# Optimization experiments

Measured on AMD Instinct MI355X. Metric: run time of the kernel, lower is better.

Reference implementation:

```python
import jax, jax.numpy as jnp
import numpy as np
from jax import lax

D, H, DK, L, FF, V, B, S = 384, 12, 32, 6, 1536, 30522, 16, 512

def _logit(p):
    return float(np.log(p / (1.0 - p)))

def setup_inputs():
    key = jax.random.key(0)
    ks = jax.random.split(key, 16)
    def g(i, shape, scale=0.02):
        return jax.random.normal(ks[i], shape, jnp.float32) * scale
    return {
        "input_ids": jax.random.randint(ks[0], (B, S), 0, V),
        "attention_mask": jnp.ones((B, S), jnp.int32),
        "emb_tok": g(1, (V, D)),
        "emb_pos": g(2, (S, D)),
        "emb_type": g(3, (2, D)),
        "emb_ln_g": jnp.ones((D,), jnp.float32),
        "emb_ln_b": jnp.zeros((D,), jnp.float32),
        "Wq": g(4, (L, D, D)), "bq": jnp.zeros((L, D), jnp.float32),
        "Wk": g(5, (L, D, D)), "bk": jnp.zeros((L, D), jnp.float32),
        "Wv": g(6, (L, D, D)), "bv": jnp.zeros((L, D), jnp.float32),
        "Wbeta": g(7, (L, D, H)), "bbeta": jnp.zeros((L, H), jnp.float32),
        "decay_fast": jnp.full((L, H), _logit(0.3), jnp.float32),
        "decay_slow": jnp.full((L, H), _logit(0.85), jnp.float32),
        "mix_logit": jnp.zeros((L, H), jnp.float32),
        "Wg": g(8, (L, D, D)),
        "Wo": g(9, (L, D, D)), "bo": jnp.zeros((L, D), jnp.float32),
        "attn_ln_g": jnp.ones((L, D), jnp.float32), "attn_ln_b": jnp.zeros((L, D), jnp.float32),
        "Wffn1": g(10, (L, D, FF)), "bffn1": jnp.zeros((L, FF), jnp.float32),
        "Wffn2": g(11, (L, FF, D)), "bffn2": jnp.zeros((L, D), jnp.float32),
        "ffn_ln_g": jnp.ones((L, D), jnp.float32), "ffn_ln_b": jnp.zeros((L, D), jnp.float32),
    }

def _ln(x, g, b, eps=1e-12):
    m = x.mean(-1, keepdims=True)
    v = ((x - m) ** 2).mean(-1, keepdims=True)
    return (x - m) * lax.rsqrt(v + eps) * g + b

def _delta_attn(x, mask_f, Wq, bq, Wk, bk, Wv, bv, Wbeta, bbeta, df_logit, ds_logit, mix_logit, Wg, Wo, bo):
    # Hierarchical delta-rule linear attention: O(n) recurrence, two decay timescales.
    Bz, Sq, _ = x.shape
    q = jax.nn.silu((x @ Wq + bq).reshape(Bz, Sq, H, DK))
    k = jax.nn.silu((x @ Wk + bk).reshape(Bz, Sq, H, DK))
    k = k / (jnp.linalg.norm(k, axis=-1, keepdims=True) + 1e-6)
    v = (x @ Wv + bv).reshape(Bz, Sq, H, DK)
    beta = jax.nn.sigmoid(x @ Wbeta + bbeta) * mask_f[..., None]  # [B,S,H]
    df = jax.nn.sigmoid(df_logit)[None, :, None, None]  # fast decay, per head
    ds = jax.nn.sigmoid(ds_logit)[None, :, None, None]  # slow decay, per head
    qT = q.transpose(1, 0, 2, 3)  # time-major [S,B,H,DK]
    kT = k.transpose(1, 0, 2, 3)
    vT = v.transpose(1, 0, 2, 3)
    betaT = beta.transpose(1, 0, 2)

    def step(carry, xs):
        Sf, Ss = carry  # [B,H,DK,DK] fast/slow memory states
        kt, vt, qt, bt = xs
        err_f = (vt - jnp.einsum('bhk,bhkv->bhv', kt, Sf)) * bt[..., None]
        Sf = df * Sf + jnp.einsum('bhk,bhv->bhkv', kt, err_f)
        err_s = (vt - jnp.einsum('bhk,bhkv->bhv', kt, Ss)) * bt[..., None]
        Ss = ds * Ss + jnp.einsum('bhk,bhv->bhkv', kt, err_s)
        of = jnp.einsum('bhk,bhkv->bhv', qt, Sf)
        os = jnp.einsum('bhk,bhkv->bhv', qt, Ss)
        return (Sf, Ss), (of, os)

    S0 = jnp.zeros((Bz, H, DK, DK), x.dtype)
    _, (ofT, osT) = lax.scan(step, (S0, S0), (kT, vT, qT, betaT))
    mix = jax.nn.sigmoid(mix_logit)[None, None, :, None]
    o = mix * ofT.transpose(1, 0, 2, 3) + (1.0 - mix) * osT.transpose(1, 0, 2, 3)
    o = o.reshape(Bz, Sq, D)
    o = o * jax.nn.sigmoid(x @ Wg)  # enhanced-flux output gate
    return o @ Wo + bo

def reference(input_ids, attention_mask, emb_tok, emb_pos, emb_type, emb_ln_g, emb_ln_b, Wq, bq, Wk, bk, Wv, bv, Wbeta, bbeta, decay_fast, decay_slow, mix_logit, Wg, Wo, bo, attn_ln_g, attn_ln_b, Wffn1, bffn1, Wffn2, bffn2, ffn_ln_g, ffn_ln_b):
    mask_f = attention_mask.astype(jnp.float32)
    h = emb_tok[input_ids] + emb_pos[None, :input_ids.shape[1]] + emb_type[0][None, None]
    h = _ln(h, emb_ln_g, emb_ln_b)
    for i in range(L):
        attn = _delta_attn(h, mask_f, Wq[i], bq[i], Wk[i], bk[i], Wv[i], bv[i], Wbeta[i], bbeta[i], decay_fast[i], decay_slow[i], mix_logit[i], Wg[i], Wo[i], bo[i])
        h = _ln(h + attn, attn_ln_g[i], attn_ln_b[i])
        ffn = jax.nn.gelu(h @ Wffn1[i] + bffn1[i], approximate=False) @ Wffn2[i] + bffn2[i]
        h = _ln(h + ffn, ffn_ln_g[i], ffn_ln_b[i])
    m = mask_f[..., None]
    emb = (h * m).sum(1) / jnp.clip(m.sum(1), 1e-9)
    return emb / (jnp.linalg.norm(emb, axis=1, keepdims=True) + 1e-12)
```

## Files before the change

### kernel.cpp

```cpp
#include <hip/hip_runtime.h>
#include <hip/hip_bf16.h>

#define NTOK   8192
#define DMODEL 384
#define NHEAD  12
#define DHEAD  32
#define NLAYER 6
#define DFF    1536
#define SEQ    512
#define BATCH  16
#define TCH    32
#define WTAL   1916928L

typedef __attribute__((ext_vector_type(8))) short short8;
typedef __attribute__((ext_vector_type(4))) float f32x4;

__device__ __forceinline__ float sigmoidf_(float x){ return 1.f/(1.f+expf(-x)); }

__device__ __forceinline__ ushort f2b(float x){
  uint b = __builtin_bit_cast(uint, x);
  uint r = (b + 0x7FFFu + ((b>>16)&1u)) >> 16;
  return (ushort)r;
}
__device__ __forceinline__ uint pk2(float lo, float hi){
  return (uint)f2b(lo) | ((uint)f2b(hi)<<16);
}
__device__ __forceinline__ float red8(float x){
  int t = __builtin_amdgcn_update_dpp(0, __builtin_bit_cast(int,x), 0xB1, 0xF, 0xF, true);
  x += __builtin_bit_cast(float,t);
  t = __builtin_amdgcn_update_dpp(0, __builtin_bit_cast(int,x), 0x4E, 0xF, 0xF, true);
  x += __builtin_bit_cast(float,t);
  t = __builtin_amdgcn_update_dpp(0, __builtin_bit_cast(int,x), 0x141, 0xF, 0xF, true);
  x += __builtin_bit_cast(float,t);
  return x;
}
__device__ __forceinline__ void gload16(const ushort* g, ushort* l){
  __builtin_amdgcn_global_load_lds((const __attribute__((address_space(1))) void*)g,
                                   (__attribute__((address_space(3))) void*)l, 16, 0, 0);
}

__global__ __launch_bounds__(128) void embed_ln_kernel(
    const int* __restrict__ ids, const float* __restrict__ tok,
    const float* __restrict__ pos, const float* __restrict__ typ,
    const float* __restrict__ g, const float* __restrict__ bvec,
    float* __restrict__ out, ushort* __restrict__ outb)
{
  int n = blockIdx.x;
  int t = n & (SEQ-1);
  int id = ids[n];
  int tid = threadIdx.x;
  float v[3]; float s1=0.f, s2=0.f;
  #pragma unroll
  for (int j=0;j<3;j++){
    int d = tid + j*128;
    float x = tok[(long)id*DMODEL + d] + pos[t*DMODEL + d] + typ[d];
    v[j]=x; s1+=x; s2+=x*x;
  }
  #pragma unroll
  for (int m=1;m<64;m<<=1){ s1 += __shfl_xor(s1,m); s2 += __shfl_xor(s2,m); }
  __shared__ float r1[2], r2[2];
  if ((tid&63)==0){ r1[tid>>6]=s1; r2[tid>>6]=s2; }
  __syncthreads();
  s1 = r1[0]+r1[1]; s2 = r2[0]+r2[1];
  float mean = s1*(1.f/DMODEL);
  float var  = s2*(1.f/DMODEL) - mean*mean;
  float inv  = rsqrtf(var + 1e-12f);
  #pragma unroll
  for (int j=0;j<3;j++){
    int d = tid + j*128;
    float y = (v[j]-mean)*inv*g[d] + bvec[d];
    out[(long)n*DMODEL + d] = y;
    outb[(long)n*DMODEL + d] = f2b(y);
  }
}

__global__ __launch_bounds__(128) void add_ln_kernel(
    float* __restrict__ h, const float* __restrict__ res,
    const float* __restrict__ g, const float* __restrict__ bvec,
    ushort* __restrict__ hb)
{
  int n = blockIdx.x;
  int tid = threadIdx.x;
  float v[3]; float s1=0.f, s2=0.f;
  #pragma unroll
  for (int j=0;j<3;j++){
    int d = tid + j*128;
    float x = h[(long)n*DMODEL + d] + res[(long)n*DMODEL + d];
    v[j]=x; s1+=x; s2+=x*x;
  }
  #pragma unroll
  for (int m=1;m<64;m<<=1){ s1 += __shfl_xor(s1,m); s2 += __shfl_xor(s2,m); }
  __shared__ float r1[2], r2[2];
  if ((tid&63)==0){ r1[tid>>6]=s1; r2[tid>>6]=s2; }
  __syncthreads();
  s1 = r1[0]+r1[1]; s2 = r2[0]+r2[1];
  float mean = s1*(1.f/DMODEL);
  float var  = s2*(1.f/DMODEL) - mean*mean;
  float inv  = rsqrtf(var + 1e-12f);
  #pragma unroll
  for (int j=0;j<3;j++){
    int d = tid + j*128;
    float y = (v[j]-mean)*inv*g[d] + bvec[d];
    h[(long)n*DMODEL + d] = y;
    hb[(long)n*DMODEL + d] = f2b(y);
  }
}

__global__ __launch_bounds__(256) void tcvt6(
    const float* __restrict__ Wq, const float* __restrict__ Wk,
    const float* __restrict__ Wv, const float* __restrict__ Wg,
    const float* __restrict__ Wo, const float* __restrict__ W1,
    const float* __restrict__ W2, ushort* __restrict__ WTA)
{
  __shared__ float tile[32][33];
  int l = blockIdx.x / 1872;
  int bid = blockIdx.x % 1872;
  const float* Wq_l = Wq + (long)l*DMODEL*DMODEL;
  const float* Wk_l = Wk + (long)l*DMODEL*DMODEL;
  const float* Wv_l = Wv + (long)l*DMODEL*DMODEL;
  const float* Wg_l = Wg + (long)l*DMODEL*DMODEL;
  const float* Wo_l = Wo + (long)l*DMODEL*DMODEL;
  const float* W1_l = W1 + (long)l*DMODEL*DFF;
  const float* W2_l = W2 + (long)l*DFF*DMODEL;
  ushort* WTAl = WTA + (long)l*WTAL;

  const float* src; long dstbase; int rowlen, Nd, tk, tn, row0;
  if (bid < 720){
    int seg = bid/144, t = bid%144;
    tk = t%12; tn = t/12;
    src = (seg==0)?Wq_l:(seg==1)?Wk_l:(seg==2)?Wv_l:(seg==3)?Wg_l:Wo_l;
    Nd = 384; rowlen = 384;
    if (seg<4){ dstbase=0; row0=seg*384; }
    else      { dstbase=589824; row0=0; }
  } else if (bid < 1296){
    int t = bid-720; tk=t%12; tn=t/12;
    src=W1_l; Nd=DFF; dstbase=737280; row0=0; rowlen=384;
  } else {
    int t = bid-1296; tk=t%48; tn=t/48;
    src=W2_l; Nd=384; dstbase=1327104; row0=0; rowlen=DFF;
  }
  int k0=tk*32, n0=tn*32;
  int tt=threadIdx.x;
  int r=tt>>3, c4=(tt&7)<<2;
  const float* sp = src + (long)(k0+r)*Nd + n0 + c4;
  float4 f = *(const float4*)sp;
  tile[r][c4+0]=f.x; tile[r][c4+1]=f.y; tile[r][c4+2]=f.z; tile[r][c4+3]=f.w;
  __syncthreads();
  ushort4 o;
  o.x=f2b(tile[c4+0][r]); o.y=f2b(tile[c4+1][r]);
  o.z=f2b(tile[c4+2][r]); o.w=f2b(tile[c4+3][r]);
  *(ushort4*)(WTAl + dstbase + (long)(row0+n0+r)*rowlen + k0 + c4) = o;
}

template<int ACT, int OUTBF>
__global__ __launch_bounds__(256) void gemm_bf(
    const ushort* __restrict__ Xb, const ushort* __restrict__ WT,
    const float* __restrict__ bias, void* __restrict__ Cv, int Kd, int Nd)
{
  __shared__ ushort A_lds[128*32];
  __shared__ ushort B_lds[128*32];
  int tid = threadIdx.x;
  int bm = blockIdx.x*128, bn = blockIdx.y*128;
  int w = tid>>6, lane = tid&63;
  int wm = w>>1, wn = w&1;
  f32x4 acc[4][4];
  #pragma unroll
  for (int i=0;i<4;i++)
    #pragma unroll
    for (int j=0;j<4;j++) acc[i][j]=(f32x4)(0.f);

  int cl = lane&15, koff = (lane>>4)*8;
  int srow = w*32 + (lane>>2);
  int scol = (lane&3)*8;
  const ushort* gA0 = Xb + (long)(bm+srow)*Kd + scol;
  const ushort* gA1 = gA0 + 16*(long)Kd;
  const ushort* gB0 = WT + (long)(bn+srow)*Kd + scol;
  const ushort* gB1 = gB0 + 16*(long)Kd;
  ushort* lA = A_lds + w*1024;
  ushort* lB = B_lds + w*1024;

  for (int k0=0; k0<Kd; k0+=32){
    gload16(gA0+k0, lA);
    gload16(gA1+k0, lA+512);
    gload16(gB0+k0, lB);
    gload16(gB1+k0, lB+512);
    __syncthreads();
    short8 bf[4];
    #pragma unroll
    for (int ni=0;ni<4;ni++)
      bf[ni] = *(const short8*)&B_lds[(wn*64+ni*16+cl)*32 + koff];
    #pragma unroll
    for (int mi=0;mi<4;mi++){
      short8 af = *(const short8*)&A_lds[(wm*64+mi*16+cl)*32 + koff];
      #pragma unroll
      for (int ni=0;ni<4;ni++)
        acc[mi][ni] = __builtin_amdgcn_mfma_f32_16x16x32_bf16(af, bf[ni], acc[mi][ni], 0,0,0);
    }
    __syncthreads();
  }

  int rb = (lane>>4)*4;
  #pragma unroll
  for (int ni=0; ni<4; ni++){
    int col = bn + wn*64 + ni*16 + cl;
    float bsv = bias ? bias[col] : 0.f;
    #pragma unroll
    for (int mi=0; mi<4; mi++){
      #pragma unroll
      for (int j=0;j<4;j++){
        int row = bm + wm*64 + mi*16 + rb + j;
        float c = acc[mi][ni][j] + bsv;
        if (ACT==1)      c = c*sigmoidf_(c);
        else if (ACT==2) c = 0.5f*c*(1.f+erff(c*0.70710678118f));
        else if (ACT==3) c = sigmoidf_(c);
        if (OUTBF) ((ushort*)Cv)[(long)row*Nd + col] = f2b(c);
        else       ((float*)Cv)[(long)row*Nd + col] = c;
      }
    }
  }
}

template<int ACT, int OUTBF>
__global__ __launch_bounds__(256) void gemm_bf2(
    const ushort* __restrict__ Xb, const ushort* __restrict__ WT,
    const float* __restrict__ bias, void* __restrict__ Cv, int Kd, int Nd)
{
  __shared__ ushort A_lds[128*32];
  __shared__ ushort B_lds[64*32];
  int tid = threadIdx.x;
  int bm = blockIdx.x*128, bn = blockIdx.y*64;
  int w = tid>>6, lane = tid&63;
  int wm = w>>1, wn = w&1;
  f32x4 acc[4][2];
  #pragma unroll
  for (int i=0;i<4;i++){ acc[i][0]=(f32x4)(0.f); acc[i][1]=(f32x4)(0.f); }

  int cl = lane&15, koff = (lane>>4)*8;
  int srowA = w*32 + (lane>>2);
  int scol = (lane&3)*8;
  const ushort* gA0 = Xb + (long)(bm+srowA)*Kd + scol;
  const ushort* gA1 = gA0 + 16*(long)Kd;
  int srowB = w*16 + (lane>>2);
  const ushort* gB = WT + (long)(bn+srowB)*Kd + scol;
  ushort* lA = A_lds + w*1024;
  ushort* lB = B_lds + w*512;

  for (int k0=0; k0<Kd; k0+=32){
    gload16(gA0+k0, lA);
    gload16(gA1+k0, lA+512);
    gload16(gB+k0, lB);
    __syncthreads();
    short8 b0 = *(const short8*)&B_lds[(wn*32+cl)*32 + koff];
    short8 b1 = *(const short8*)&B_lds[(wn*32+16+cl)*32 + koff];
    #pragma unroll
    for (int mi=0;mi<4;mi++){
      short8 af = *(const short8*)&A_lds[(wm*64+mi*16+cl)*32 + koff];
      acc[mi][0] = __builtin_amdgcn_mfma_f32_16x16x32_bf16(af, b0, acc[mi][0], 0,0,0);
      acc[mi][1] = __builtin_amdgcn_mfma_f32_16x16x32_bf16(af, b1, acc[mi][1], 0,0,0);
    }
    __syncthreads();
  }

  int rb = (lane>>4)*4;
  #pragma unroll
  for (int ni=0; ni<2; ni++){
    int col = bn + wn*32 + ni*16 + cl;
    float bsv = bias ? bias[col] : 0.f;
    #pragma unroll
    for (int mi=0; mi<4; mi++){
      #pragma unroll
      for (int j=0;j<4;j++){
        int row = bm + wm*64 + mi*16 + rb + j;
        float c = acc[mi][ni][j] + bsv;
        if (ACT==1)      c = c*sigmoidf_(c);
        else if (ACT==2) c = 0.5f*c*(1.f+erff(c*0.70710678118f));
        else if (ACT==3) c = sigmoidf_(c);
        if (OUTBF) ((ushort*)Cv)[(long)row*Nd + col] = f2b(c);
        else       ((float*)Cv)[(long)row*Nd + col] = c;
      }
    }
  }
}

__global__ __launch_bounds__(256) void gemm_qkvg(
    const ushort* __restrict__ Xb, const ushort* __restrict__ WT,
    const float* __restrict__ bq, const float* __restrict__ bk,
    const float* __restrict__ bv, float* __restrict__ C)
{
  __shared__ ushort A_lds[128*32];
  __shared__ ushort B_lds[128*32];
  int tid = threadIdx.x;
  int bm = blockIdx.x*128, bn = blockIdx.y*128;
  int w = tid>>6, lane = tid&63;
  int wm = w>>1, wn = w&1;
  f32x4 acc[4][4];
  #pragma unroll
  for (int i=0;i<4;i++)
    #pragma unroll
    for (int j=0;j<4;j++) acc[i][j]=(f32x4)(0.f);

  int cl = lane&15, koff = (lane>>4)*8;
  int srow = w*32 + (lane>>2);
  int scol = (lane&3)*8;
  const ushort* gA0 = Xb + (long)(bm+srow)*DMODEL + scol;
  const ushort* gA1 = gA0 + 16*DMODEL;
  const ushort* gB0 = WT + (long)(bn+srow)*DMODEL + scol;
  const ushort* gB1 = gB0 + 16*DMODEL;
  ushort* lA = A_lds + w*1024;
  ushort* lB = B_lds + w*1024;

  for (int k0=0; k0<DMODEL; k0+=32){
    gload16(gA0+k0, lA);
    gload16(gA1+k0, lA+512);
    gload16(gB0+k0, lB);
    gload16(gB1+k0, lB+512);
    __syncthreads();
    short8 bf[4];
    #pragma unroll
    for (int ni=0;ni<4;ni++)
      bf[ni] = *(const short8*)&B_lds[(wn*64+ni*16+cl)*32 + koff];
    #pragma unroll
    for (int mi=0;mi<4;mi++){
      short8 af = *(const short8*)&A_lds[(wm*64+mi*16+cl)*32 + koff];
      #pragma unroll
      for (int ni=0;ni<4;ni++)
        acc[mi][ni] = __builtin_amdgcn_mfma_f32_16x16x32_bf16(af, bf[ni], acc[mi][ni], 0,0,0);
    }
    __syncthreads();
  }

  int seg = blockIdx.y/3;
  const float* bp = (seg==0)?bq:(seg==1)?bk:(seg==2)?bv:nullptr;
  int boff = seg*384;
  int rb = (lane>>4)*4;
  #pragma unroll
  for (int ni=0; ni<4; ni++){
    int col = bn + wn*64 + ni*16 + cl;
    float bsv = bp ? bp[col-boff] : 0.f;
    #pragma unroll
    for (int mi=0; mi<4; mi++){
      #pragma unroll
      for (int j=0;j<4;j++){
        int row = bm + wm*64 + mi*16 + rb + j;
        float c = acc[mi][ni][j] + bsv;
        if (seg<2)       c = c*sigmoidf_(c);
        else if (seg==3) c = sigmoidf_(c);
        C[(long)row*DFF + col] = c;
      }
    }
  }
}

__global__ __launch_bounds__(384) void aux_kernel(
    float* __restrict__ QKVG, const float* __restrict__ X,
    const float* __restrict__ Wb, const float* __restrict__ bb,
    const int* __restrict__ mask, float* __restrict__ Bb)
{
  int bid = blockIdx.x;
  int tid = threadIdx.x;
  if (bid < NTOK){
    long a = (long)bid*DFF + 384 + tid;
    float x = QKVG[a];
    float ss = x*x;
    #pragma unroll
    for (int m=1;m<32;m<<=1) ss += __shfl_xor(ss,m);
    QKVG[a] = x / (sqrtf(ss)+1e-6f);
  } else {
    int n = bid - NTOK;
    __shared__ float xs[DMODEL];
    xs[tid] = X[(long)n*DMODEL + tid];
    __syncthreads();
    int hh = tid >> 5, i = tid & 31;
    float s = 0.f;
    for (int d=i; d<DMODEL; d+=32) s += xs[d]*Wb[d*NHEAD+hh];
    #pragma unroll
    for (int m=1;m<32;m<<=1) s += __shfl_xor(s,m);
    if (i==0) Bb[n*NHEAD+hh] = (float)mask[n] * sigmoidf_(s + bb[hh]);
  }
}

__global__ __launch_bounds__(512,2) void scan8_kernel(
    const float* __restrict__ QKVG, const float* __restrict__ Bb,
    const float* __restrict__ dfl, const float* __restrict__ dsl,
    const float* __restrict__ mixl, ushort* __restrict__ OA)
{
  __shared__ float Qc[2][TCH][36], Kc[2][TCH][36], Vc[2][TCH][36];
  __shared__ float Bc[2][TCH];
  __shared__ float Ofs[2][TCH][36];
  int bh = blockIdx.x;
  int b = bh / NHEAD, hh = bh - b*NHEAD;
  int tid = threadIdx.x;
  int w = tid>>6, lane = tid&63;
  int st = w>>2, vq = w&3;
  int kq = lane&7, v = vq*8 + (lane>>3);
  float dec = sigmoidf_(st ? dsl[hh] : dfl[hh]);
  float mix = sigmoidf_(mixl[hh]);
  long rowbase = (long)b*SEQ;
  const float* rp = QKVG + rowbase*DFF + hh*32;
  const float* bp = Bb + rowbase*NHEAD + hh;

  int rem0 = tid & 255, r0 = rem0>>3, c40 = (rem0&7)<<2;
  bool isK = tid >= 256;
  int brow = tid - 480;
  int et = tid>>3, ev0 = (tid&7)<<2;

  float S[4] = {0.f,0.f,0.f,0.f};

  {
    float4 a0 = *(const float4*)(rp + (long)r0*DFF + (isK?384:0) + c40);
    float4 v0m = a0;
    if (!isK) v0m = *(const float4*)(rp + (long)r0*DFF + 768 + c40);
    float bb0 = 0.f;
    if (tid>=480) bb0 = bp[(long)brow*NHEAD];
    if (isK) *(float4*)&Kc[0][r0][c40] = a0;
    else { *(float4*)&Qc[0][r0][c40] = a0; *(float4*)&Vc[0][r0][c40] = v0m; }
    if (tid>=480) Bc[0][brow] = bb0;
  }
  __syncthreads();

  for (int c=0; c<SEQ/TCH; ++c){
    int cur = c&1;
    float4 nA, nV; float nB = 0.f;
    if (c+1 < SEQ/TCH){
      long rb2 = (long)((c+1)*TCH + r0)*DFF;
      nA = *(const float4*)(rp + rb2 + (isK?384:0) + c40);
      if (!isK) nV = *(const float4*)(rp + rb2 + 768 + c40);
      if (tid>=480) nB = bp[(long)((c+1)*TCH + brow)*NHEAD];
    }
    float4 g4;
    if (tid<256)
      g4 = *(const float4*)(QKVG + (rowbase + c*TCH + et)*DFF + 1152 + hh*32 + ev0);

    float4 k4 = *(const float4*)&Kc[cur][0][kq*4];
    float4 q4 = *(const float4*)&Qc[cur][0][kq*4];
    float vt = Vc[cur][0][v];
    float bt = Bc[cur][0];
    #pragma unroll 4
    for (int t=0; t<TCH; ++t){
      int tn = (t+1<TCH)?(t+1):t;
      float4 k4n = *(const float4*)&Kc[cur][tn][kq*4];
      float4 q4n = *(const float4*)&Qc[cur][tn][kq*4];
      float vn = Vc[cur][tn][v];
      float bn = Bc[cur][tn];
      float pa = k4.x*S[0] + k4.y*S[1];
      float pb = k4.z*S[2] + k4.w*S[3];
      float p = red8(pa+pb);
      float err = (vt - p)*bt;
      S[0] = dec*S[0] + k4.x*err;
      S[1] = dec*S[1] + k4.y*err;
      S[2] = dec*S[2] + k4.z*err;
      S[3] = dec*S[3] + k4.w*err;
      float oa = q4.x*S[0] + q4.y*S[1];
      float ob = q4.z*S[2] + q4.w*S[3];
      float o = red8(oa+ob);
      if (kq==0) Ofs[st][t][v] = o;
      k4=k4n; q4=q4n; vt=vn; bt=bn;
    }
    if (c+1 < SEQ/TCH){
      int nxt = (c+1)&1;
      if (isK) *(float4*)&Kc[nxt][r0][c40] = nA;
      else { *(float4*)&Qc[nxt][r0][c40] = nA; *(float4*)&Vc[nxt][r0][c40] = nV; }
      if (tid>=480) Bc[nxt][brow] = nB;
    }
    __syncthreads();
    if (tid < 256){
      long r = rowbase + c*TCH + et;
      float4 of = *(const float4*)&Ofs[0][et][ev0];
      float4 os = *(const float4*)&Ofs[1][et][ev0];
      float a0 = (mix*of.x + (1.f-mix)*os.x)*g4.x;
      float a1 = (mix*of.y + (1.f-mix)*os.y)*g4.y;
      float a2 = (mix*of.z + (1.f-mix)*os.z)*g4.z;
      float a3 = (mix*of.w + (1.f-mix)*os.w)*g4.w;
      uint2 o2; o2.x = pk2(a0,a1); o2.y = pk2(a2,a3);
      *(uint2*)(OA + r*DMODEL + hh*32 + ev0) = o2;
    }
    __syncthreads();
  }
}

__global__ __launch_bounds__(384) void pool_norm_kernel(
    const float* __restrict__ h, const int* __restrict__ mask, float* __restrict__ out)
{
  int b = blockIdx.x; int d = threadIdx.x;
  float s=0.f, ms=0.f;
  for (int t=0;t<SEQ;t++){
    float m = (float)mask[b*SEQ+t];
    s += h[((long)b*SEQ+t)*DMODEL + d]*m;
    ms += m;
  }
  float emb = s / fmaxf(ms, 1e-9f);
  float ss = emb*emb;
  #pragma unroll
  for (int m2=1;m2<64;m2<<=1) ss += __shfl_xor(ss,m2);
  __shared__ float r[6];
  if ((d&63)==0) r[d>>6]=ss;
  __syncthreads();
  ss = r[0]+r[1]+r[2]+r[3]+r[4]+r[5];
  out[b*DMODEL+d] = emb / (sqrtf(ss)+1e-12f);
}

extern "C" void kernel_launch(void* const* d_in, const int* in_sizes, int n_in,
                              void* d_out, int out_size, void* d_ws, size_t ws_size,
                              hipStream_t stream)
{
  const int*   ids   = (const int*)d_in[0];
  const int*   amask = (const int*)d_in[1];
  const float* etok  = (const float*)d_in[2];
  const float* epos  = (const float*)d_in[3];
  const float* etyp  = (const float*)d_in[4];
  const float* elng  = (const float*)d_in[5];
  const float* elnb  = (const float*)d_in[6];
  const float* Wq = (const float*)d_in[7];  const float* bq = (const float*)d_in[8];
  const float* Wk = (const float*)d_in[9];  const float* bk = (const float*)d_in[10];
  const float* Wv = (const float*)d_in[11]; const float* bv = (const float*)d_in[12];
  const float* Wb = (const float*)d_in[13]; const float* bb = (const float*)d_in[14];
  const float* dfl = (const float*)d_in[15];
  const float* dsl = (const float*)d_in[16];
  const float* mixl= (const float*)d_in[17];
  const float* Wg = (const float*)d_in[18];
  const float* Wo = (const float*)d_in[19]; const float* bo = (const float*)d_in[20];
  const float* alng = (const float*)d_in[21]; const float* alnb = (const float*)d_in[22];
  const float* W1 = (const float*)d_in[23]; const float* b1 = (const float*)d_in[24];
  const float* W2 = (const float*)d_in[25]; const float* b2 = (const float*)d_in[26];
  const float* flng = (const float*)d_in[27]; const float* flnb = (const float*)d_in[28];

  float* ws = (float*)d_ws;
  const long TD = (long)NTOK*DMODEL;
  float* h    = ws;
  ushort* hbf = (ushort*)(h + TD);
  float* QKVG = h + TD + TD/2;
  ushort* OA  = (ushort*)(QKVG + 4*TD);
  float* Rb   = QKVG + 4*TD + TD/2;
  float* Bb   = Rb + TD;
  ushort* WTA = (ushort*)(Bb + (long)NTOK*NHEAD);
  ushort* F1B = (ushort*)QKVG;

  embed_ln_kernel<<<NTOK,128,0,stream>>>(ids, etok, epos, etyp, elng, elnb, h, hbf);
  tcvt6<<<6*1872,256,0,stream>>>(Wq, Wk, Wv, Wg, Wo, W1, W2, WTA);

  for (int l=0;l<NLAYER;l++){
    ushort* WTAl = WTA + (long)l*WTAL;
    gemm_qkvg<<<dim3(64,12),256,0,stream>>>(hbf, WTAl, bq+l*DMODEL, bk+l*DMODEL, bv+l*DMODEL, QKVG);
    aux_kernel<<<2*NTOK,384,0,stream>>>(QKVG, h, Wb + (long)l*DMODEL*NHEAD, bb + l*NHEAD, amask, Bb);
    scan8_kernel<<<BATCH*NHEAD,512,0,stream>>>(QKVG, Bb, dfl + l*NHEAD, dsl + l*NHEAD, mixl + l*NHEAD, OA);
    gemm_bf2<0,0><<<dim3(64,6),256,0,stream>>>(OA, WTAl+589824, bo + l*DMODEL, Rb, DMODEL, DMODEL);
    add_ln_kernel<<<NTOK,128,0,stream>>>(h, Rb, alng + (long)l*DMODEL, alnb + (long)l*DMODEL, hbf);
    gemm_bf<2,1><<<dim3(64,12),256,0,stream>>>(hbf, WTAl+737280, b1 + (long)l*DFF, F1B, DMODEL, DFF);
    gemm_bf2<0,0><<<dim3(64,6),256,0,stream>>>(F1B, WTAl+1327104, b2 + (long)l*DMODEL, Rb, DFF, DMODEL);
    add_ln_kernel<<<NTOK,128,0,stream>>>(h, Rb, flng + (long)l*DMODEL, flnb + (long)l*DMODEL, hbf);
  }

  pool_norm_kernel<<<BATCH,384,0,stream>>>(h, amask, (float*)d_out);
}
```

Baseline: 1.416 ms.

## Fuse key normalization into scan, enlarge scan chunks, and XCD-swizzle GEMM blocks

The k-vector L2 normalization moves from the auxiliary kernel into the scan kernel's chunk loader, so a full read-modify-write pass over the K slice of QKVG is gone and the aux kernel shrinks to a beta-only kernel. The scan now processes 64-token chunks (8 per sequence instead of 16), which halves the number of barriers. V is stored transposed in LDS and V and beta are read as float4 groups of four timesteps. GEMM kernels also remap block indices so blocks that run on the same XCD share tiles for better L2 locality. In exchange the scan uses more LDS and single-buffered staging, which may expose load latency.

```diff
diff --git a/kernel.cpp b/kernel.cpp
--- a/kernel.cpp
+++ b/kernel.cpp
@@ -9,7 +9,6 @@
 #define DFF    1536
 #define SEQ    512
 #define BATCH  16
-#define TCH    32
 #define WTAL   1916928L
 
 typedef __attribute__((ext_vector_type(8))) short short8;
@@ -152,6 +151,13 @@
   *(ushort4*)(WTAl + dstbase + (long)(row0+n0+r)*rowlen + k0 + c4) = o;
 }
 
+__device__ __forceinline__ int2 xcd_swz(){
+  int lin = blockIdx.y*64 + blockIdx.x;
+  int nb = gridDim.x*gridDim.y;
+  int s = (lin & 7)*(nb>>3) + (lin>>3);
+  return make_int2(s & 63, s >> 6);
+}
+
 template<int ACT, int OUTBF>
 __global__ __launch_bounds__(256) void gemm_bf(
     const ushort* __restrict__ Xb, const ushort* __restrict__ WT,
@@ -160,7 +166,8 @@
   __shared__ ushort A_lds[128*32];
   __shared__ ushort B_lds[128*32];
   int tid = threadIdx.x;
-  int bm = blockIdx.x*128, bn = blockIdx.y*128;
+  int2 bxy = xcd_swz();
+  int bm = bxy.x*128, bn = bxy.y*128;
   int w = tid>>6, lane = tid&63;
   int wm = w>>1, wn = w&1;
   f32x4 acc[4][4];
@@ -228,7 +235,8 @@
   __shared__ ushort A_lds[128*32];
   __shared__ ushort B_lds[64*32];
   int tid = threadIdx.x;
-  int bm = blockIdx.x*128, bn = blockIdx.y*64;
+  int2 bxy = xcd_swz();
+  int bm = bxy.x*128, bn = bxy.y*64;
   int w = tid>>6, lane = tid&63;
   int wm = w>>1, wn = w&1;
   f32x4 acc[4][2];
@@ -290,7 +298,8 @@
   __shared__ ushort A_lds[128*32];
   __shared__ ushort B_lds[128*32];
   int tid = threadIdx.x;
-  int bm = blockIdx.x*128, bn = blockIdx.y*128;
+  int2 bxy = xcd_swz();
+  int bm = bxy.x*128, bn = bxy.y*128;
   int w = tid>>6, lane = tid&63;
   int wm = w>>1, wn = w&1;
   f32x4 acc[4][4];
@@ -329,7 +338,7 @@
     __syncthreads();
   }
 
-  int seg = blockIdx.y/3;
+  int seg = bxy.y/3;
   const float* bp = (seg==0)?bq:(seg==1)?bk:(seg==2)?bv:nullptr;
   int boff = seg*384;
   int rb = (lane>>4)*4;
@@ -351,42 +360,28 @@
   }
 }
 
-__global__ __launch_bounds__(384) void aux_kernel(
-    float* __restrict__ QKVG, const float* __restrict__ X,
-    const float* __restrict__ Wb, const float* __restrict__ bb,
+__global__ __launch_bounds__(384) void beta_kernel(
+    const float* __restrict__ X, const float* __restrict__ Wb, const float* __restrict__ bb,
     const int* __restrict__ mask, float* __restrict__ Bb)
 {
-  int bid = blockIdx.x;
-  int tid = threadIdx.x;
-  if (bid < NTOK){
-    long a = (long)bid*DFF + 384 + tid;
-    float x = QKVG[a];
-    float ss = x*x;
-    #pragma unroll
-    for (int m=1;m<32;m<<=1) ss += __shfl_xor(ss,m);
-    QKVG[a] = x / (sqrtf(ss)+1e-6f);
-  } else {
-    int n = bid - NTOK;
-    __shared__ float xs[DMODEL];
-    xs[tid] = X[(long)n*DMODEL + tid];
-    __syncthreads();
-    int hh = tid >> 5, i = tid & 31;
-    float s = 0.f;
-    for (int d=i; d<DMODEL; d+=32) s += xs[d]*Wb[d*NHEAD+hh];
-    #pragma unroll
-    for (int m=1;m<32;m<<=1) s += __shfl_xor(s,m);
-    if (i==0) Bb[n*NHEAD+hh] = (float)mask[n] * sigmoidf_(s + bb[hh]);
-  }
-}
-
-__global__ __launch_bounds__(512,2) void scan8_kernel(
+  __shared__ float xs[DMODEL];
+  int n = blockIdx.x; int tid = threadIdx.x;
+  xs[tid] = X[(long)n*DMODEL + tid];
+  __syncthreads();
+  int hh = tid >> 5, i = tid & 31;
+  float s = 0.f;
+  for (int d=i; d<DMODEL; d+=32) s += xs[d]*Wb[d*NHEAD+hh];
+  #pragma unroll
+  for (int m=1;m<32;m<<=1) s += __shfl_xor(s,m);
+  if (i==0) Bb[n*NHEAD+hh] = (float)mask[n] * sigmoidf_(s + bb[hh]);
+}
+
+__global__ __launch_bounds__(512,2) void scan9_kernel(
     const float* __restrict__ QKVG, const float* __restrict__ Bb,
     const float* __restrict__ dfl, const float* __restrict__ dsl,
     const float* __restrict__ mixl, ushort* __restrict__ OA)
 {
-  __shared__ float Qc[2][TCH][36], Kc[2][TCH][36], Vc[2][TCH][36];
-  __shared__ float Bc[2][TCH];
-  __shared__ float Ofs[2][TCH][36];
+  __shared__ float Qc[65][36], Kc[65][36], Vt[32][68], Bc[64], Ofs[2][64][36];
   int bh = blockIdx.x;
   int b = bh / NHEAD, hh = bh - b*NHEAD;
   int tid = threadIdx.x;
@@ -399,80 +394,81 @@
   const float* rp = QKVG + rowbase*DFF + hh*32;
   const float* bp = Bb + rowbase*NHEAD + hh;
 
-  int rem0 = tid & 255, r0 = rem0>>3, c40 = (rem0&7)<<2;
-  bool isK = tid >= 256;
-  int brow = tid - 480;
-  int et = tid>>3, ev0 = (tid&7)<<2;
-
+  int r0 = tid>>3, c40 = (tid&7)<<2;
   float S[4] = {0.f,0.f,0.f,0.f};
 
+  float4 sq, sk, sv; float sb = 0.f;
   {
-    float4 a0 = *(const float4*)(rp + (long)r0*DFF + (isK?384:0) + c40);
-    float4 v0m = a0;
-    if (!isK) v0m = *(const float4*)(rp + (long)r0*DFF + 768 + c40);
-    float bb0 = 0.f;
-    if (tid>=480) bb0 = bp[(long)brow*NHEAD];
-    if (isK) *(float4*)&Kc[0][r0][c40] = a0;
-    else { *(float4*)&Qc[0][r0][c40] = a0; *(float4*)&Vc[0][r0][c40] = v0m; }
-    if (tid>=480) Bc[0][brow] = bb0;
+    long g = (long)r0*DFF;
+    sq = *(const float4*)(rp + g + c40);
+    sk = *(const float4*)(rp + g + 384 + c40);
+    sv = *(const float4*)(rp + g + 768 + c40);
+    if (tid < 64) sb = bp[(long)tid*NHEAD];
+    float ss = red8(sk.x*sk.x + sk.y*sk.y + sk.z*sk.z + sk.w*sk.w);
+    float inv = 1.f/(sqrtf(ss)+1e-6f);
+    sk.x*=inv; sk.y*=inv; sk.z*=inv; sk.w*=inv;
+    *(float4*)&Qc[r0][c40] = sq;
+    *(float4*)&Kc[r0][c40] = sk;
+    Vt[c40+0][r0]=sv.x; Vt[c40+1][r0]=sv.y; Vt[c40+2][r0]=sv.z; Vt[c40+3][r0]=sv.w;
+    if (tid < 64) Bc[tid] = sb;
   }
   __syncthreads();
 
-  for (int c=0; c<SEQ/TCH; ++c){
-    int cur = c&1;
-    float4 nA, nV; float nB = 0.f;
-    if (c+1 < SEQ/TCH){
-      long rb2 = (long)((c+1)*TCH + r0)*DFF;
-      nA = *(const float4*)(rp + rb2 + (isK?384:0) + c40);
-      if (!isK) nV = *(const float4*)(rp + rb2 + 768 + c40);
-      if (tid>=480) nB = bp[(long)((c+1)*TCH + brow)*NHEAD];
-    }
-    float4 g4;
-    if (tid<256)
-      g4 = *(const float4*)(QKVG + (rowbase + c*TCH + et)*DFF + 1152 + hh*32 + ev0);
-
-    float4 k4 = *(const float4*)&Kc[cur][0][kq*4];
-    float4 q4 = *(const float4*)&Qc[cur][0][kq*4];
-    float vt = Vc[cur][0][v];
-    float bt = Bc[cur][0];
-    #pragma unroll 4
-    for (int t=0; t<TCH; ++t){
-      int tn = (t+1<TCH)?(t+1):t;
-      float4 k4n = *(const float4*)&Kc[cur][tn][kq*4];
-      float4 q4n = *(const float4*)&Qc[cur][tn][kq*4];
-      float vn = Vc[cur][tn][v];
-      float bn = Bc[cur][tn];
-      float pa = k4.x*S[0] + k4.y*S[1];
-      float pb = k4.z*S[2] + k4.w*S[3];
-      float p = red8(pa+pb);
-      float err = (vt - p)*bt;
-      S[0] = dec*S[0] + k4.x*err;
-      S[1] = dec*S[1] + k4.y*err;
-      S[2] = dec*S[2] + k4.z*err;
-      S[3] = dec*S[3] + k4.w*err;
-      float oa = q4.x*S[0] + q4.y*S[1];
-      float ob = q4.z*S[2] + q4.w*S[3];
-      float o = red8(oa+ob);
-      if (kq==0) Ofs[st][t][v] = o;
-      k4=k4n; q4=q4n; vt=vn; bt=bn;
-    }
-    if (c+1 < SEQ/TCH){
-      int nxt = (c+1)&1;
-      if (isK) *(float4*)&Kc[nxt][r0][c40] = nA;
-      else { *(float4*)&Qc[nxt][r0][c40] = nA; *(float4*)&Vc[nxt][r0][c40] = nV; }
-      if (tid>=480) Bc[nxt][brow] = nB;
-    }
-    __syncthreads();
-    if (tid < 256){
-      long r = rowbase + c*TCH + et;
-      float4 of = *(const float4*)&Ofs[0][et][ev0];
-      float4 os = *(const float4*)&Ofs[1][et][ev0];
+  for (int c=0; c<8; ++c){
+    if (c < 7){
+      long g = (long)((c+1)*64 + r0)*DFF;
+      sq = *(const float4*)(rp + g + c40);
+      sk = *(const float4*)(rp + g + 384 + c40);
+      sv = *(const float4*)(rp + g + 768 + c40);
+      if (tid < 64) sb = bp[(long)((c+1)*64 + tid)*NHEAD];
+    }
+    float4 g4 = *(const float4*)(rp + (long)(c*64 + r0)*DFF + 1152 + c40);
+
+    float4 k4 = *(const float4*)&Kc[0][kq*4];
+    float4 q4 = *(const float4*)&Qc[0][kq*4];
+    for (int t4=0; t4<16; ++t4){
+      float br[4]; *(float4*)br = *(const float4*)&Bc[t4*4];
+      float vr[4]; *(float4*)vr = *(const float4*)&Vt[v][t4*4];
+      #pragma unroll
+      for (int i=0;i<4;i++){
+        int t = t4*4 + i;
+        float4 k4n = *(const float4*)&Kc[t+1][kq*4];
+        float4 q4n = *(const float4*)&Qc[t+1][kq*4];
+        float pa = k4.x*S[0] + k4.y*S[1];
+        float pb = k4.z*S[2] + k4.w*S[3];
+        float p = red8(pa+pb);
+        float err = (vr[i] - p)*br[i];
+        S[0] = dec*S[0] + k4.x*err;
+        S[1] = dec*S[1] + k4.y*err;
+        S[2] = dec*S[2] + k4.z*err;
+        S[3] = dec*S[3] + k4.w*err;
+        float oa = q4.x*S[0] + q4.y*S[1];
+        float ob = q4.z*S[2] + q4.w*S[3];
+        float o = red8(oa+ob);
+        if (kq==0) Ofs[st][t][v] = o;
+        k4=k4n; q4=q4n;
+      }
+    }
+    __syncthreads();
+
+    {
+      float4 of = *(const float4*)&Ofs[0][r0][c40];
+      float4 os = *(const float4*)&Ofs[1][r0][c40];
       float a0 = (mix*of.x + (1.f-mix)*os.x)*g4.x;
       float a1 = (mix*of.y + (1.f-mix)*os.y)*g4.y;
       float a2 = (mix*of.z + (1.f-mix)*os.z)*g4.z;
       float a3 = (mix*of.w + (1.f-mix)*os.w)*g4.w;
       uint2 o2; o2.x = pk2(a0,a1); o2.y = pk2(a2,a3);
-      *(uint2*)(OA + r*DMODEL + hh*32 + ev0) = o2;
+      *(uint2*)(OA + (rowbase + c*64 + r0)*DMODEL + hh*32 + c40) = o2;
+    }
+    if (c < 7){
+      float ss = red8(sk.x*sk.x + sk.y*sk.y + sk.z*sk.z + sk.w*sk.w);
+      float inv = 1.f/(sqrtf(ss)+1e-6f);
+      sk.x*=inv; sk.y*=inv; sk.z*=inv; sk.w*=inv;
+      *(float4*)&Qc[r0][c40] = sq;
+      *(float4*)&Kc[r0][c40] = sk;
+      Vt[c40+0][r0]=sv.x; Vt[c40+1][r0]=sv.y; Vt[c40+2][r0]=sv.z; Vt[c40+3][r0]=sv.w;
+      if (tid < 64) Bc[tid] = sb;
     }
     __syncthreads();
   }
@@ -541,8 +537,8 @@
   for (int l=0;l<NLAYER;l++){
     ushort* WTAl = WTA + (long)l*WTAL;
     gemm_qkvg<<<dim3(64,12),256,0,stream>>>(hbf, WTAl, bq+l*DMODEL, bk+l*DMODEL, bv+l*DMODEL, QKVG);
-    aux_kernel<<<2*NTOK,384,0,stream>>>(QKVG, h, Wb + (long)l*DMODEL*NHEAD, bb + l*NHEAD, amask, Bb);
-    scan8_kernel<<<BATCH*NHEAD,512,0,stream>>>(QKVG, Bb, dfl + l*NHEAD, dsl + l*NHEAD, mixl + l*NHEAD, OA);
+    beta_kernel<<<NTOK,384,0,stream>>>(h, Wb + (long)l*DMODEL*NHEAD, bb + l*NHEAD, amask, Bb);
+    scan9_kernel<<<BATCH*NHEAD,512,0,stream>>>(QKVG, Bb, dfl + l*NHEAD, dsl + l*NHEAD, mixl + l*NHEAD, OA);
     gemm_bf2<0,0><<<dim3(64,6),256,0,stream>>>(OA, WTAl+589824, bo + l*DMODEL, Rb, DMODEL, DMODEL);
     add_ln_kernel<<<NTOK,128,0,stream>>>(h, Rb, alng + (long)l*DMODEL, alnb + (long)l*DMODEL, hbf);
     gemm_bf<2,1><<<dim3(64,12),256,0,stream>>>(hbf, WTAl+737280, b1 + (long)l*DFF, F1B, DMODEL, DFF);
```

Result: faster. 1.369 ms (-3.3%).
